# Optimization experiments

Measured on AMD Instinct MI355X. Metric: run time of the kernel, lower is better.

## Reference

```python
import jax, jax.numpy as jnp
import numpy as np

B, D, H, O, E = 16384, 1024, 512, 256, 8


def setup_inputs() -> dict:
    key = jax.random.key(0)
    ks = jax.random.split(key, 8)
    s = lambda k, shape, fan: (jax.random.normal(k, shape, jnp.float32) / np.sqrt(fan).astype(np.float32))
    z = lambda shape: jnp.zeros(shape, jnp.float32)
    return {
        "x": jax.random.normal(ks[0], (B, D), jnp.float32),
        # gating network: D -> 256 -> 128 -> E
        "gw1": s(ks[1], (D, 256), D), "gb1": z((256,)),
        "gw2": s(ks[2], (256, 128), 256), "gb2": z((128,)),
        "gw3": s(ks[3], (128, E), 128), "gb3": z((E,)),
        # experts, batched over expert dim E: D -> H -> H -> O
        "ew1": s(ks[4], (E, D, H), D), "eb1": z((E, H)),
        "ew2": s(ks[5], (E, H, H), H), "eb2": z((E, H)),
        "ew3": s(ks[6], (E, H, O), H), "eb3": z((E, O)),
    }


def reference(x, gw1, gb1, gw2, gb2, gw3, gb3, ew1, eb1, ew2, eb2, ew3, eb3):
    # Gating network (dropout is identity in eval mode)
    g = jax.nn.relu(x @ gw1 + gb1)
    g = jax.nn.relu(g @ gw2 + gb2)
    gates = jax.nn.softmax(g @ gw3 + gb3, axis=1)  # [B, E]
    # All experts run on every token: batched small MLPs over expert axis e
    h = jax.nn.relu(jnp.einsum('bd,edh->ebh', x, ew1) + eb1[:, None, :])   # [E, B, H]
    h = jax.nn.relu(jnp.einsum('ebh,ehk->ebk', h, ew2) + eb2[:, None, :])  # [E, B, H]
    eo = jnp.einsum('ebh,eho->ebo', h, ew3) + eb3[:, None, :]              # [E, B, O]
    # gate-weighted sum over experts
    out = jnp.einsum('ebo,be->bo', eo, gates)  # [B, O]
    return out
```

## Files before the change

### kernel.cpp

```cpp
#include <hip/hip_runtime.h>
#include <hip/hip_bf16.h>

typedef __hip_bfloat16 bf16;
typedef __attribute__((ext_vector_type(8))) __bf16 bf16x8;
typedef __attribute__((ext_vector_type(4))) float f32x4;

#define B_ 16384
#define D_ 1024
#define H_ 512
#define O_ 256
#define E_ 8
#define BC_ 8192

static_assert(B_ % BC_ == 0, "chunking");

#define GLDS(src, dst) __builtin_amdgcn_global_load_lds( \
    (const __attribute__((address_space(1))) void*)(src), \
    (__attribute__((address_space(3))) void*)(dst), 16, 0, 0)

#define BAR()   asm volatile("s_barrier" ::: "memory")
#define LGKM0() do { asm volatile("s_waitcnt lgkmcnt(0)" ::: "memory"); \
                     __builtin_amdgcn_sched_barrier(0); } while (0)

__global__ void detect_k(const unsigned short* __restrict__ x, int* __restrict__ flag) {
    __shared__ int s;
    if (threadIdx.x == 0) s = 0;
    __syncthreads();
    int big = 0;
    for (int i = threadIdx.x; i < 2048; i += 256)
        if (((x[i] >> 7) & 0xFF) >= 150) big = 1;
    if (big) atomicOr(&s, 1);
    __syncthreads();
    if (threadIdx.x == 0) *flag = s;
}

__global__ void cvtx_k(const void* __restrict__ src, bf16* __restrict__ dst,
                       const int* __restrict__ flag, long n8) {
    const int f = *flag;
    long i = (long)blockIdx.x * blockDim.x + threadIdx.x;
    const long stride = (long)gridDim.x * blockDim.x;
    if (f) {
        const float4* s = (const float4*)src;
        for (; i < n8; i += stride) {
            float4 a = s[2 * i], b = s[2 * i + 1];
            bf16 tmp[8];
            tmp[0] = __float2bfloat16(a.x); tmp[1] = __float2bfloat16(a.y);
            tmp[2] = __float2bfloat16(a.z); tmp[3] = __float2bfloat16(a.w);
            tmp[4] = __float2bfloat16(b.x); tmp[5] = __float2bfloat16(b.y);
            tmp[6] = __float2bfloat16(b.z); tmp[7] = __float2bfloat16(b.w);
            *(uint4*)(dst + i * 8) = *(const uint4*)tmp;
        }
    } else {
        const uint4* s = (const uint4*)src;
        for (; i < n8; i += stride) *(uint4*)(dst + i * 8) = s[i];
    }
}

__global__ void small_cvt_k(const void* s0, const void* s1, const void* s2,
                            const void* s3, const void* s4, const void* s5,
                            const void* s6,
                            bf16* d0, bf16* d1, bf16* d2, bf16* d3,
                            bf16* d4, bf16* d5, bf16* d6,
                            const int* __restrict__ flag) {
    const int f = *flag;
    const int id = blockIdx.x;
    const void* sp[7] = {s0, s1, s2, s3, s4, s5, s6};
    bf16* dp[7] = {d0, d1, d2, d3, d4, d5, d6};
    const int len[7] = {256, 128, 1024, 8, E_ * H_, E_ * H_, E_ * O_};
    const float* sf = (const float*)sp[id];
    const bf16*  sb = (const bf16*)sp[id];
    bf16* d = dp[id];
    for (int i = threadIdx.x; i < len[id]; i += 256)
        d[i] = f ? __float2bfloat16(sf[i]) : sb[i];
}

__global__ void transpose_all_k(const void* gw1, const void* gw2,
                                const void* ew1, const void* ew2, const void* ew3,
                                bf16* gw1t, bf16* gw2t,
                                bf16* ew1t, bf16* ew2t, bf16* ew3t,
                                long ew3_zout, long ew3_cstride,
                                const int* __restrict__ flag) {
    __shared__ bf16 t[32][33];
    const int f = *flag;
    int lin = blockIdx.x;
    const void* src; bf16* dst; int R, C, bx, by, bz; long z_out, c_stride;
    if (lin < 256) {
        src = gw1; dst = gw1t; R = 1024; C = 256; z_out = 0; c_stride = 1024;
        bx = lin & 7; by = lin >> 3; bz = 0;
    } else if (lin < 288) {
        lin -= 256;
        src = gw2; dst = gw2t; R = 256; C = 128; z_out = 0; c_stride = 256;
        bx = lin & 3; by = lin >> 2; bz = 0;
    } else if (lin < 4384) {
        lin -= 288;
        src = ew1; dst = ew1t; R = 1024; C = 512;
        z_out = (long)H_ * D_; c_stride = D_;
        bx = lin & 15; by = (lin >> 4) & 31; bz = lin >> 9;
    } else if (lin < 6432) {
        lin -= 4384;
        src = ew2; dst = ew2t; R = 512; C = 512;
        z_out = (long)H_ * H_; c_stride = H_;
        bx = lin & 15; by = (lin >> 4) & 15; bz = lin >> 8;
    } else {
        lin -= 6432;
        src = ew3; dst = ew3t; R = 512; C = 256;
        z_out = ew3_zout; c_stride = ew3_cstride;
        bx = lin & 7; by = (lin >> 3) & 15; bz = lin >> 7;
    }
    const long zi = (long)bz * R * C;
    const int x = bx * 32 + threadIdx.x;
    const int y0 = by * 32;
    const float* inf = (const float*)src;
    const bf16* inb = (const bf16*)src;
#pragma unroll
    for (int i = 0; i < 4; i++) {
        int r = y0 + threadIdx.y + i * 8;
        long idx = zi + (long)r * C + x;
        t[threadIdx.y + i * 8][threadIdx.x] =
            f ? __float2bfloat16(inf[idx]) : inb[idx];
    }
    __syncthreads();
    const int xr = by * 32 + threadIdx.x;
    const long zo = (long)bz * z_out;
#pragma unroll
    for (int i = 0; i < 4; i++) {
        int c = bx * 32 + threadIdx.y + i * 8;
        dst[zo + (long)c * c_stride + xr] = t[threadIdx.x][threadIdx.y + i * 8];
    }
}

__global__ void gate3_softmax_k(const bf16* __restrict__ g2,
                                const bf16* __restrict__ gw3,
                                const bf16* __restrict__ gb3,
                                float* __restrict__ gates) {
    __shared__ float w[128 * 8];
    __shared__ float bsh[8];
    const int tid = threadIdx.x;
    for (int i = tid; i < 1024; i += 256) w[i] = __bfloat162float(gw3[i]);
    if (tid < 8) bsh[tid] = __bfloat162float(gb3[tid]);
    __syncthreads();

    const long row = (long)blockIdx.x * 256 + tid;
    float acc[8];
#pragma unroll
    for (int o = 0; o < 8; o++) acc[o] = bsh[o];

    const bf16x8* rp8 = (const bf16x8*)(g2 + row * 128);
#pragma unroll 4
    for (int c8 = 0; c8 < 16; c8++) {
        bf16x8 v8 = rp8[c8];
#pragma unroll
        for (int jj = 0; jj < 8; jj++) {
            float v = (float)v8[jj];
            int k = c8 * 8 + jj;
#pragma unroll
            for (int o = 0; o < 8; o++) acc[o] += v * w[k * 8 + o];
        }
    }
    float m = acc[0];
#pragma unroll
    for (int o = 1; o < 8; o++) m = fmaxf(m, acc[o]);
    float s = 0.f;
#pragma unroll
    for (int o = 0; o < 8; o++) { acc[o] = __expf(acc[o] - m); s += acc[o]; }
    const float inv = 1.f / s;
#pragma unroll
    for (int o = 0; o < 8; o++) gates[row * 8 + o] = acc[o] * inv;
}

template <int MODE>
__global__ __launch_bounds__(256, 4)
void gemm_bt(const bf16* __restrict__ A, const bf16* __restrict__ Bt,
             const bf16* __restrict__ bias, const float* __restrict__ gates,
             void* __restrict__ Cout, const bf16* __restrict__ eb3,
             int lda, int ldb, int ldo, int K,
             long a_z, long b_z, long bias_z, long out_z,
             int e_gate, int k_per_e, long a_e, long b_e, long row0) {
    __shared__ __attribute__((aligned(16))) bf16 As[128 * 32];
    __shared__ __attribute__((aligned(16))) bf16 Bs[128 * 32];

    const int tid  = threadIdx.x;
    const int lane = tid & 63;
    const int quad = lane >> 4;
    const int l15  = lane & 15;
    const int wid  = tid >> 6;
    const int wr   = (wid >> 1) << 6;
    const int wc   = (wid & 1) << 6;
    const int z    = blockIdx.z;
    const long m0  = (long)blockIdx.y << 7;
    const long n0  = (long)blockIdx.x << 7;

    const bf16* Az = A + (long)z * a_z;
    const bf16* Bz = Bt + (long)z * b_z;

    f32x4 acc[4][4];
#pragma unroll
    for (int i = 0; i < 4; i++)
#pragma unroll
        for (int j = 0; j < 4; j++) acc[i][j] = (f32x4){0.f, 0.f, 0.f, 0.f};

    const int erow = tid >> 2;
    const int ecol = (tid & 3) << 3;

    const int n_e   = k_per_e ? (K / k_per_e) : 1;
    const int inner = (k_per_e ? k_per_e : K) >> 5;

    for (int e = 0; e < n_e; e++) {
        const bf16* Ae = Az + (long)e * a_e;
        const bf16* Be = Bz + (long)e * b_e;
        for (int kti = 0; kti < inner; kti++) {
            const int kk = kti << 5;
#pragma unroll
            for (int i = 0; i < 2; i++) {
                const int r = (i << 6) + erow;
                GLDS(Ae + (m0 + r) * lda + (kk + ecol), As + r * 32 + ecol);
            }
#pragma unroll
            for (int i = 0; i < 2; i++) {
                const int r = (i << 6) + erow;
                GLDS(Be + (n0 + r) * ldb + (kk + ecol), Bs + r * 32 + ecol);
            }
            __syncthreads();
            bf16x8 af[4], bfr[4];
#pragma unroll
            for (int i = 0; i < 4; i++)
                af[i] = *(const bf16x8*)(As + (wr + i * 16 + l15) * 32 + (quad << 3));
#pragma unroll
            for (int j = 0; j < 4; j++)
                bfr[j] = *(const bf16x8*)(Bs + (wc + j * 16 + l15) * 32 + (quad << 3));
#pragma unroll
            for (int i = 0; i < 4; i++)
#pragma unroll
                for (int j = 0; j < 4; j++)
                    acc[i][j] = __builtin_amdgcn_mfma_f32_16x16x32_bf16(
                        af[i], bfr[j], acc[i][j], 0, 0, 0);
            __syncthreads();
        }
    }

    const int eg = (e_gate >= 0) ? e_gate : z;

    if constexpr (MODE == 0 || MODE == 1) {
        bf16* C = (bf16*)Cout + (long)z * out_z;
        const bf16* bb = bias + (long)z * bias_z;
        float gv[4][4];
        if constexpr (MODE == 1) {
#pragma unroll
            for (int i = 0; i < 4; i++)
#pragma unroll
                for (int rg = 0; rg < 4; rg++)
                    gv[i][rg] = gates[(row0 + m0 + wr + i * 16 + quad * 4 + rg) * 8 + eg];
        }
#pragma unroll
        for (int j = 0; j < 4; j++) {
            const int c = (int)n0 + wc + j * 16 + l15;
            const float bv = __bfloat162float(bb[c]);
#pragma unroll
            for (int i = 0; i < 4; i++) {
#pragma unroll
                for (int rg = 0; rg < 4; rg++) {
                    const long r = m0 + wr + i * 16 + quad * 4 + rg;
                    float v = fmaxf(acc[i][j][rg] + bv, 0.f);
                    if constexpr (MODE == 1) v *= gv[i][rg];
                    C[r * ldo + c] = __float2bfloat16(v);
                }
            }
        }
    } else if constexpr (MODE == 2) {
        float* C = (float*)Cout;
#pragma unroll
        for (int i = 0; i < 4; i++) {
#pragma unroll
            for (int rg = 0; rg < 4; rg++) {
                const long r = m0 + wr + i * 16 + quad * 4 + rg;
                const float g = gates[(row0 + r) * 8 + eg];
#pragma unroll
                for (int j = 0; j < 4; j++) {
                    const int c = (int)n0 + wc + j * 16 + l15;
                    const float b3 = __bfloat162float(eb3[eg * O_ + c]);
                    C[r * ldo + c] += acc[i][j][rg] + g * b3;
                }
            }
        }
    }
}

template <int MODE>
__global__ __launch_bounds__(512, 2)
void gemm256(const bf16* __restrict__ A, const bf16* __restrict__ Bt,
             const bf16* __restrict__ bias, const float* __restrict__ gates,
             void* __restrict__ Cout, const bf16* __restrict__ eb3,
             int lda, int ldb, int ldo, int K,
             long a_z, long b_z, long bias_z, long out_z, long row0) {
    __shared__ __attribute__((aligned(16))) bf16 lds[2][2][256 * 64];

    int bx = blockIdx.x, by = blockIdx.y;
    {
        const int gx = gridDim.x;
        const int nwg = gx * gridDim.y;
        if ((nwg & 7) == 0) {
            int lin = bx + gx * by;
            lin = (lin & 7) * (nwg >> 3) + (lin >> 3);
            bx = lin % gx; by = lin / gx;
        }
    }

    const int tid  = threadIdx.x;
    const int lane = tid & 63;
    const int quad = lane >> 4;
    const int l15  = lane & 15;
    const int w    = tid >> 6;
    const int wm   = w >> 2;
    const int wn   = w & 3;
    const int z    = blockIdx.z;
    const long m0  = (long)by << 8;
    const long n0  = (long)bx << 8;

    const bf16* __restrict__ Az = A + z * a_z;
    const bf16* __restrict__ Bz = Bt + z * b_z;

    f32x4 acc[8][4];
#pragma unroll
    for (int i = 0; i < 8; ++i)
#pragma unroll
        for (int j = 0; j < 4; ++j) acc[i][j] = (f32x4){0.f, 0.f, 0.f, 0.f};

    bf16x8 af[4][2], bv[2][2];

    auto stage = [&](int buf, int mat, int half, int kt) {
        const bf16* __restrict__ G = mat ? Bz : Az;
        const int ld = mat ? ldb : lda;
        const long p0 = mat ? n0 : m0;
#pragma unroll
        for (int l = 0; l < 2; ++l) {
            const int ci = (w << 1) | l;
            const int rb = mat ? ((ci >> 2) << 6) + (half << 5) + ((ci & 3) << 3)
                               : ((ci >> 3) << 7) + (half << 6) + ((ci & 7) << 3);
            const int row = rb + (lane >> 3);
            const int cb  = ((lane & 7) << 4) ^ ((row & 7) << 4);
            GLDS(G + (p0 + row) * ld + kt * 64 + (cb >> 1),
                 &lds[buf][mat][rb * 64]);
        }
    };
    auto ldaf = [&](int buf, int qm) {
#pragma unroll
        for (int i = 0; i < 4; ++i) {
            const int r = (wm << 7) + (qm << 6) + (i << 4) + l15;
            const char* p = (const char*)&lds[buf][0][r * 64];
            const int sw = (r & 7) << 4;
#pragma unroll
            for (int s = 0; s < 2; ++s)
                af[i][s] = *(const bf16x8*)(p + (((s << 6) + (quad << 4)) ^ sw));
        }
    };
    auto ldbf = [&](int buf, int qn) {
#pragma unroll
        for (int j = 0; j < 2; ++j) {
            const int r = (wn << 6) + (qn << 5) + (j << 4) + l15;
            const char* p = (const char*)&lds[buf][1][r * 64];
            const int sw = (r & 7) << 4;
#pragma unroll
            for (int s = 0; s < 2; ++s)
                bv[j][s] = *(const bf16x8*)(p + (((s << 6) + (quad << 4)) ^ sw));
        }
    };
    auto mmac = [&](int qm, int qn) {
#pragma unroll
        for (int i = 0; i < 4; ++i)
#pragma unroll
            for (int j = 0; j < 2; ++j)
#pragma unroll
                for (int s = 0; s < 2; ++s)
                    acc[(qm << 2) + i][(qn << 1) + j] =
                        __builtin_amdgcn_mfma_f32_16x16x32_bf16(
                            af[i][s], bv[j][s], acc[(qm << 2) + i][(qn << 1) + j],
                            0, 0, 0);
    };

    const int nt = K >> 6;

    stage(0, 0, 0, 0); stage(0, 0, 1, 0); stage(0, 1, 0, 0); stage(0, 1, 1, 0);
    stage(1, 0, 0, 1); stage(1, 1, 0, 1);
    asm volatile("s_waitcnt vmcnt(4)" ::: "memory");
    BAR();

    const int hi = nt >> 1;
    for (int it = 0; it < hi; ++it) {
        const int t1k = 2 * it + 1, t2k = 2 * it + 2, t3k = 2 * it + 3;
        const bool do2 = t2k < nt, do3 = t3k < nt;
        ldaf(0, 0); ldbf(0, 0); stage(1, 0, 1, t1k);
        BAR(); LGKM0();
        __builtin_amdgcn_s_setprio(1); mmac(0, 0); __builtin_amdgcn_s_setprio(0);
        BAR();
        ldbf(0, 1); stage(1, 1, 1, t1k);
        BAR(); LGKM0();
        __builtin_amdgcn_s_setprio(1); mmac(0, 1); __builtin_amdgcn_s_setprio(0);
        BAR();
        ldaf(0, 1); ldbf(0, 0); if (do2) stage(0, 0, 0, t2k);
        BAR(); LGKM0();
        __builtin_amdgcn_s_setprio(1); mmac(1, 0); __builtin_amdgcn_s_setprio(0);
        BAR();
        ldbf(0, 1); if (do2) stage(0, 1, 0, t2k);
        BAR(); LGKM0();
        __builtin_amdgcn_s_setprio(1); mmac(1, 1); __builtin_amdgcn_s_setprio(0);
        if (do2) { asm volatile("s_waitcnt vmcnt(4)" ::: "memory"); }
        else     { asm volatile("s_waitcnt vmcnt(0)" ::: "memory"); }
        BAR();
        ldaf(1, 0); ldbf(1, 0); if (do2) stage(0, 0, 1, t2k);
        BAR(); LGKM0();
        __builtin_amdgcn_s_setprio(1); mmac(0, 0); __builtin_amdgcn_s_setprio(0);
        BAR();
        ldbf(1, 1); if (do2) stage(0, 1, 1, t2k);
        BAR(); LGKM0();
        __builtin_amdgcn_s_setprio(1); mmac(0, 1); __builtin_amdgcn_s_setprio(0);
        BAR();
        ldaf(1, 1); ldbf(1, 0); if (do3) stage(1, 0, 0, t3k);
        BAR(); LGKM0();
        __builtin_amdgcn_s_setprio(1); mmac(1, 0); __builtin_amdgcn_s_setprio(0);
        BAR();
        ldbf(1, 1); if (do3) stage(1, 1, 0, t3k);
        BAR(); LGKM0();
        __builtin_amdgcn_s_setprio(1); mmac(1, 1); __builtin_amdgcn_s_setprio(0);
        if (do3) { asm volatile("s_waitcnt vmcnt(4)" ::: "memory"); }
        else     { asm volatile("s_waitcnt vmcnt(0)" ::: "memory"); }
        BAR();
    }

    if constexpr (MODE == 0 || MODE == 1) {
        bf16* C = (bf16*)Cout + z * out_z;
        const bf16* bb = bias + z * bias_z;
        float bvv[4];
#pragma unroll
        for (int jg = 0; jg < 4; ++jg)
            bvv[jg] = __bfloat162float(bb[(int)n0 + (wn << 6) + (jg << 4) + l15]);
#pragma unroll
        for (int ig = 0; ig < 8; ++ig) {
#pragma unroll
            for (int rg = 0; rg < 4; ++rg) {
                const long r = m0 + (wm << 7) + (ig << 4) + (quad << 2) + rg;
                float g = 1.f;
                if constexpr (MODE == 1) g = gates[(row0 + r) * 8 + z];
#pragma unroll
                for (int jg = 0; jg < 4; ++jg) {
                    const int c = (int)n0 + (wn << 6) + (jg << 4) + l15;
                    float v = fmaxf(acc[ig][jg][rg] + bvv[jg], 0.f);
                    if constexpr (MODE == 1) v *= g;
                    C[r * ldo + c] = __float2bfloat16(v);
                }
            }
        }
    } else if constexpr (MODE == 4) {
        float* C = (float*)Cout + z * out_z;
        float b3v[4];
#pragma unroll
        for (int jg = 0; jg < 4; ++jg)
            b3v[jg] = __bfloat162float(eb3[z * O_ + (int)n0 + (wn << 6) + (jg << 4) + l15]);
#pragma unroll
        for (int ig = 0; ig < 8; ++ig) {
#pragma unroll
            for (int rg = 0; rg < 4; ++rg) {
                const long r = m0 + (wm << 7) + (ig << 4) + (quad << 2) + rg;
                const float g = gates[(row0 + r) * 8 + z];
#pragma unroll
                for (int jg = 0; jg < 4; ++jg) {
                    const int c = (int)n0 + (wn << 6) + (jg << 4) + l15;
                    C[r * ldo + c] = acc[ig][jg][rg] + g * b3v[jg];
                }
            }
        }
    } else {
        float* C = (float*)Cout + z * out_z;
        const int e0 = z << 1;
        float b30[4], b31[4];
#pragma unroll
        for (int jg = 0; jg < 4; ++jg) {
            const int c = (int)n0 + (wn << 6) + (jg << 4) + l15;
            b30[jg] = __bfloat162float(eb3[e0 * O_ + c]);
            b31[jg] = __bfloat162float(eb3[(e0 + 1) * O_ + c]);
        }
#pragma unroll
        for (int ig = 0; ig < 8; ++ig) {
#pragma unroll
            for (int rg = 0; rg < 4; ++rg) {
                const long r = m0 + (wm << 7) + (ig << 4) + (quad << 2) + rg;
                const float g0 = gates[(row0 + r) * 8 + e0];
                const float g1 = gates[(row0 + r) * 8 + e0 + 1];
#pragma unroll
                for (int jg = 0; jg < 4; ++jg) {
                    const int c = (int)n0 + (wn << 6) + (jg << 4) + l15;
                    C[r * ldo + c] = acc[ig][jg][rg] + g0 * b30[jg] + g1 * b31[jg];
                }
            }
        }
    }
}

__global__ void zero_f32_k(float* __restrict__ p) {
    p[(long)blockIdx.x * 256 + threadIdx.x] = 0.f;
}
__global__ void out_cvt_k(const float* __restrict__ in, void* __restrict__ out,
                          const int* __restrict__ flag) {
    const long i = (long)blockIdx.x * 256 + threadIdx.x;
    if (*flag) ((float*)out)[i] = in[i];
    else       ((bf16*)out)[i] = __float2bfloat16(in[i]);
}
template <int NZ>
__global__ void reduceN_k(const float* __restrict__ p, void* __restrict__ out,
                          const int* __restrict__ flag, long n, long off) {
    const long i = ((long)blockIdx.x * 256 + threadIdx.x) * 4;
    float4 s = *(const float4*)(p + i);
#pragma unroll
    for (int zz = 1; zz < NZ; ++zz) {
        float4 a = *(const float4*)(p + (long)zz * n + i);
        s.x += a.x; s.y += a.y; s.z += a.z; s.w += a.w;
    }
    if (*flag) {
        *(float4*)((float*)out + off + i) = s;
    } else {
        bf16* o = (bf16*)out + off + i;
        o[0] = __float2bfloat16(s.x); o[1] = __float2bfloat16(s.y);
        o[2] = __float2bfloat16(s.z); o[3] = __float2bfloat16(s.w);
    }
}

extern "C" void kernel_launch(void* const* d_in, const int* in_sizes, int n_in,
                              void* d_out, int out_size, void* d_ws, size_t ws_size,
                              hipStream_t stream) {
    (void)in_sizes; (void)n_in; (void)out_size;
    const void* x   = d_in[0];
    const void* gw1 = d_in[1];
    const void* gb1 = d_in[2];
    const void* gw2 = d_in[3];
    const void* gb2 = d_in[4];
    const void* gw3 = d_in[5];
    const void* gb3 = d_in[6];
    const void* ew1 = d_in[7];
    const void* eb1 = d_in[8];
    const void* ew2 = d_in[9];
    const void* eb2 = d_in[10];
    const void* ew3 = d_in[11];
    const void* eb3 = d_in[12];

    char* ws = (char*)d_ws;
    size_t off = 0;
    auto alloc = [&](size_t n) { char* p = ws + off; off += (n + 255) & ~(size_t)255; return p; };

    int*  flag  = (int*)alloc(256);
    bf16* xc    = (bf16*)alloc((size_t)B_ * D_ * 2);
    bf16* gw1t  = (bf16*)alloc((size_t)256 * 1024 * 2);
    bf16* gw2t  = (bf16*)alloc((size_t)128 * 256 * 2);
    bf16* ew1t  = (bf16*)alloc((size_t)E_ * H_ * D_ * 2);
    bf16* ew2t  = (bf16*)alloc((size_t)E_ * H_ * H_ * 2);
    bf16* ew3t  = (bf16*)alloc((size_t)E_ * O_ * H_ * 2);
    bf16* gb1c  = (bf16*)alloc(256 * 2);
    bf16* gb2c  = (bf16*)alloc(128 * 2);
    bf16* gw3c  = (bf16*)alloc(1024 * 2);
    bf16* gb3c  = (bf16*)alloc(8 * 2);
    bf16* eb1c  = (bf16*)alloc((size_t)E_ * H_ * 2);
    bf16* eb2c  = (bf16*)alloc((size_t)E_ * H_ * 2);
    bf16* eb3c  = (bf16*)alloc((size_t)E_ * O_ * 2);
    bf16* g1    = (bf16*)alloc((size_t)B_ * 256 * 2);
    bf16* g2b   = (bf16*)alloc((size_t)B_ * 128 * 2);
    float* gates = (float*)alloc((size_t)B_ * 8 * 4);

    const size_t small = off;
    const size_t needPair = small + ((size_t)E_ * BC_ * H_ * 2 + 256)
                                  + ((size_t)B_ * E_ * H_ * 2 + 256)
                                  + (4ull * B_ * O_ * 4 + 256) + 4096;
    const size_t needChunk = small + ((size_t)E_ * BC_ * H_ * 2 + 256)
                                   + ((size_t)BC_ * E_ * H_ * 2 + 256)
                                   + (8ull * BC_ * O_ * 4 + 256) + 4096;
    const bool pathPair  = ws_size >= needPair;
    const bool pathChunk = ws_size >= needChunk;

    detect_k<<<1, 256, 0, stream>>>((const unsigned short*)x, flag);

    cvtx_k<<<1024, 256, 0, stream>>>(x, xc, flag, (long)B_ * D_ / 8);
    small_cvt_k<<<7, 256, 0, stream>>>(gb1, gb2, gw3, gb3, eb1, eb2, eb3,
                                       gb1c, gb2c, gw3c, gb3c, eb1c, eb2c, eb3c,
                                       flag);

    const long e3zo = pathChunk ? (long)H_ : (long)O_ * H_;
    const long e3cs = pathChunk ? (long)E_ * H_ : (long)H_;
    transpose_all_k<<<7456, dim3(32, 8), 0, stream>>>(
        gw1, gw2, ew1, ew2, ew3, gw1t, gw2t, ew1t, ew2t, ew3t, e3zo, e3cs, flag);

    gemm_bt<0><<<dim3(2, 128, 1), 256, 0, stream>>>(
        xc, gw1t, gb1c, nullptr, g1, nullptr,
        1024, 1024, 256, 1024, 0, 0, 0, 0, 0, 0, 0, 0, 0);
    gemm_bt<0><<<dim3(1, 128, 1), 256, 0, stream>>>(
        g1, gw2t, gb2c, nullptr, g2b, nullptr,
        256, 256, 128, 256, 0, 0, 0, 0, 0, 0, 0, 0, 0);
    gate3_softmax_k<<<dim3(B_ / 256), 256, 0, stream>>>(g2b, gw3c, gb3c, gates);

    if (pathChunk) {
        bf16* h1c = (bf16*)alloc((size_t)E_ * BC_ * H_ * 2);
        bf16* h2  = pathPair
                  ? (bf16*)alloc((size_t)B_ * E_ * H_ * 2)
                  : (bf16*)alloc((size_t)BC_ * E_ * H_ * 2);
        float* parts = pathPair
                     ? (float*)alloc(4ull * B_ * O_ * 4)
                     : (float*)alloc(8ull * BC_ * O_ * 4);

        for (int ch = 0; ch < B_ / BC_; ch++) {
            const long rb = (long)ch * BC_;
            gemm256<0><<<dim3(2, BC_ / 256, 8), 512, 0, stream>>>(
                xc + rb * D_, ew1t, eb1c, nullptr, h1c, nullptr,
                D_, D_, H_, D_,
                0, (long)H_ * D_, (long)H_, (long)BC_ * H_, 0);
            bf16* h2dst = pathPair ? (h2 + rb * (long)E_ * H_) : h2;
            gemm256<1><<<dim3(2, BC_ / 256, 8), 512, 0, stream>>>(
                h1c, ew2t, eb2c, gates, h2dst, nullptr,
                H_, H_, E_ * H_, H_,
                (long)BC_ * H_, (long)H_ * H_, (long)H_, (long)H_, rb);
            if (!pathPair) {
                gemm256<4><<<dim3(1, BC_ / 256, 8), 512, 0, stream>>>(
                    h2, ew3t, nullptr, gates, parts, eb3c,
                    E_ * H_, E_ * H_, O_, 512,
                    (long)H_, (long)H_, 0, (long)BC_ * O_, rb);
                reduceN_k<8><<<dim3(BC_ * O_ / 1024), 256, 0, stream>>>(
                    parts, d_out, flag, (long)BC_ * O_, rb * O_);
            }
        }
        if (pathPair) {
            gemm256<5><<<dim3(1, B_ / 256, 4), 512, 0, stream>>>(
                h2, ew3t, nullptr, gates, parts, eb3c,
                E_ * H_, E_ * H_, O_, 1024,
                2L * H_, 2L * H_, 0, (long)B_ * O_, 0);
            reduceN_k<4><<<dim3(B_ * O_ / 1024), 256, 0, stream>>>(
                parts, d_out, flag, (long)B_ * O_, 0L);
        }
    } else {
        bf16* h1s = (bf16*)alloc((size_t)B_ * H_ * 2);
        bf16* h2s = (bf16*)alloc((size_t)B_ * H_ * 2);
        float* oacc = (float*)alloc((size_t)B_ * O_ * 4);
        zero_f32_k<<<dim3(B_ * O_ / 256), 256, 0, stream>>>(oacc);
        for (int e = 0; e < E_; e++) {
            gemm_bt<0><<<dim3(4, 128, 1), 256, 0, stream>>>(
                xc, ew1t + (size_t)e * H_ * D_, eb1c + (size_t)e * H_, nullptr, h1s, nullptr,
                1024, 1024, 512, 1024, 0, 0, 0, 0, 0, 0, 0, 0, 0);
            gemm_bt<1><<<dim3(4, 128, 1), 256, 0, stream>>>(
                h1s, ew2t + (size_t)e * H_ * H_, eb2c + (size_t)e * H_, gates, h2s, nullptr,
                512, 512, 512, 512, 0, 0, 0, 0, e, 0, 0, 0, 0);
            gemm_bt<2><<<dim3(2, 128, 1), 256, 0, stream>>>(
                h2s, ew3t + (size_t)e * O_ * H_, nullptr, gates, oacc, eb3c,
                512, 512, 256, 512, 0, 0, 0, 0, e, 0, 0, 0, 0);
        }
        out_cvt_k<<<dim3(B_ * O_ / 256), 256, 0, stream>>>(oacc, d_out, flag);
    }
}
```

Baseline: 532.9 us.

## Fuse expert-3 GEMM over all experts with K=4096 and direct output write

The third expert layer used to produce per-expert or per-pair fp32 partial outputs plus a separate reduction kernel. It now runs one gemm_bt over the concatenated expert dimension (K = E*H). The gate-weighted biases are applied in the epilogue, and the result goes straight to the output in fp32 or bf16. When the workspace allows, the chunk loop is also collapsed into one full-batch pass. This drops the partials buffer and reduce kernel at the cost of a single long-K GEMM on the smaller 128-tile kernel, which may have lower throughput than gemm256.

```diff
diff --git a/kernel.cpp b/kernel.cpp
--- a/kernel.cpp
+++ b/kernel.cpp
@@ -173,6 +173,7 @@
 void gemm_bt(const bf16* __restrict__ A, const bf16* __restrict__ Bt,
              const bf16* __restrict__ bias, const float* __restrict__ gates,
              void* __restrict__ Cout, const bf16* __restrict__ eb3,
+             const int* __restrict__ oflag,
              int lda, int ldb, int ldo, int K,
              long a_z, long b_z, long bias_z, long out_z,
              int e_gate, int k_per_e, long a_e, long b_e, long row0) {
@@ -282,6 +283,36 @@
                 }
             }
         }
+    } else {
+        const int f = *oflag;
+        float b3[4][8];
+#pragma unroll
+        for (int j = 0; j < 4; j++) {
+            const int c = (int)n0 + wc + j * 16 + l15;
+#pragma unroll
+            for (int e = 0; e < 8; e++)
+                b3[j][e] = __bfloat162float(eb3[e * O_ + c]);
+        }
+#pragma unroll
+        for (int i = 0; i < 4; i++) {
+#pragma unroll
+            for (int rg = 0; rg < 4; rg++) {
+                const long r = row0 + m0 + wr + i * 16 + quad * 4 + rg;
+                const float4* gp = (const float4*)(gates + r * 8);
+                const float4 ga = gp[0], gb = gp[1];
+#pragma unroll
+                for (int j = 0; j < 4; j++) {
+                    const int c = (int)n0 + wc + j * 16 + l15;
+                    float v = acc[i][j][rg]
+                            + ga.x * b3[j][0] + ga.y * b3[j][1]
+                            + ga.z * b3[j][2] + ga.w * b3[j][3]
+                            + gb.x * b3[j][4] + gb.y * b3[j][5]
+                            + gb.z * b3[j][6] + gb.w * b3[j][7];
+                    if (f) ((float*)Cout)[r * ldo + c] = v;
+                    else   ((bf16*)Cout)[r * ldo + c] = __float2bfloat16(v);
+                }
+            }
+        }
     }
 }
 
@@ -426,70 +457,25 @@
         BAR();
     }
 
-    if constexpr (MODE == 0 || MODE == 1) {
-        bf16* C = (bf16*)Cout + z * out_z;
-        const bf16* bb = bias + z * bias_z;
-        float bvv[4];
-#pragma unroll
-        for (int jg = 0; jg < 4; ++jg)
-            bvv[jg] = __bfloat162float(bb[(int)n0 + (wn << 6) + (jg << 4) + l15]);
-#pragma unroll
-        for (int ig = 0; ig < 8; ++ig) {
-#pragma unroll
-            for (int rg = 0; rg < 4; ++rg) {
-                const long r = m0 + (wm << 7) + (ig << 4) + (quad << 2) + rg;
-                float g = 1.f;
-                if constexpr (MODE == 1) g = gates[(row0 + r) * 8 + z];
-#pragma unroll
-                for (int jg = 0; jg < 4; ++jg) {
-                    const int c = (int)n0 + (wn << 6) + (jg << 4) + l15;
-                    float v = fmaxf(acc[ig][jg][rg] + bvv[jg], 0.f);
-                    if constexpr (MODE == 1) v *= g;
-                    C[r * ldo + c] = __float2bfloat16(v);
-                }
-            }
-        }
-    } else if constexpr (MODE == 4) {
-        float* C = (float*)Cout + z * out_z;
-        float b3v[4];
-#pragma unroll
-        for (int jg = 0; jg < 4; ++jg)
-            b3v[jg] = __bfloat162float(eb3[z * O_ + (int)n0 + (wn << 6) + (jg << 4) + l15]);
-#pragma unroll
-        for (int ig = 0; ig < 8; ++ig) {
-#pragma unroll
-            for (int rg = 0; rg < 4; ++rg) {
-                const long r = m0 + (wm << 7) + (ig << 4) + (quad << 2) + rg;
-                const float g = gates[(row0 + r) * 8 + z];
-#pragma unroll
-                for (int jg = 0; jg < 4; ++jg) {
-                    const int c = (int)n0 + (wn << 6) + (jg << 4) + l15;
-                    C[r * ldo + c] = acc[ig][jg][rg] + g * b3v[jg];
-                }
-            }
-        }
-    } else {
-        float* C = (float*)Cout + z * out_z;
-        const int e0 = z << 1;
-        float b30[4], b31[4];
-#pragma unroll
-        for (int jg = 0; jg < 4; ++jg) {
-            const int c = (int)n0 + (wn << 6) + (jg << 4) + l15;
-            b30[jg] = __bfloat162float(eb3[e0 * O_ + c]);
-            b31[jg] = __bfloat162float(eb3[(e0 + 1) * O_ + c]);
-        }
-#pragma unroll
-        for (int ig = 0; ig < 8; ++ig) {
-#pragma unroll
-            for (int rg = 0; rg < 4; ++rg) {
-                const long r = m0 + (wm << 7) + (ig << 4) + (quad << 2) + rg;
-                const float g0 = gates[(row0 + r) * 8 + e0];
-                const float g1 = gates[(row0 + r) * 8 + e0 + 1];
-#pragma unroll
-                for (int jg = 0; jg < 4; ++jg) {
-                    const int c = (int)n0 + (wn << 6) + (jg << 4) + l15;
-                    C[r * ldo + c] = acc[ig][jg][rg] + g0 * b30[jg] + g1 * b31[jg];
-                }
+    bf16* C = (bf16*)Cout + z * out_z;
+    const bf16* bb = bias + z * bias_z;
+    float bvv[4];
+#pragma unroll
+    for (int jg = 0; jg < 4; ++jg)
+        bvv[jg] = __bfloat162float(bb[(int)n0 + (wn << 6) + (jg << 4) + l15]);
+#pragma unroll
+    for (int ig = 0; ig < 8; ++ig) {
+#pragma unroll
+        for (int rg = 0; rg < 4; ++rg) {
+            const long r = m0 + (wm << 7) + (ig << 4) + (quad << 2) + rg;
+            float g = 1.f;
+            if constexpr (MODE == 1) g = gates[(row0 + r) * 8 + z];
+#pragma unroll
+            for (int jg = 0; jg < 4; ++jg) {
+                const int c = (int)n0 + (wn << 6) + (jg << 4) + l15;
+                float v = fmaxf(acc[ig][jg][rg] + bvv[jg], 0.f);
+                if constexpr (MODE == 1) v *= g;
+                C[r * ldo + c] = __float2bfloat16(v);
             }
         }
     }
@@ -503,24 +489,6 @@
     const long i = (long)blockIdx.x * 256 + threadIdx.x;
     if (*flag) ((float*)out)[i] = in[i];
     else       ((bf16*)out)[i] = __float2bfloat16(in[i]);
-}
-template <int NZ>
-__global__ void reduceN_k(const float* __restrict__ p, void* __restrict__ out,
-                          const int* __restrict__ flag, long n, long off) {
-    const long i = ((long)blockIdx.x * 256 + threadIdx.x) * 4;
-    float4 s = *(const float4*)(p + i);
-#pragma unroll
-    for (int zz = 1; zz < NZ; ++zz) {
-        float4 a = *(const float4*)(p + (long)zz * n + i);
-        s.x += a.x; s.y += a.y; s.z += a.z; s.w += a.w;
-    }
-    if (*flag) {
-        *(float4*)((float*)out + off + i) = s;
-    } else {
-        bf16* o = (bf16*)out + off + i;
-        o[0] = __float2bfloat16(s.x); o[1] = __float2bfloat16(s.y);
-        o[2] = __float2bfloat16(s.z); o[3] = __float2bfloat16(s.w);
-    }
 }
 
 extern "C" void kernel_launch(void* const* d_in, const int* in_sizes, int n_in,
@@ -564,13 +532,11 @@
     float* gates = (float*)alloc((size_t)B_ * 8 * 4);
 
     const size_t small = off;
-    const size_t needPair = small + ((size_t)E_ * BC_ * H_ * 2 + 256)
-                                  + ((size_t)B_ * E_ * H_ * 2 + 256)
-                                  + (4ull * B_ * O_ * 4 + 256) + 4096;
+    const size_t needBig = small + ((size_t)E_ * B_ * H_ * 2 + 256)
+                                 + ((size_t)B_ * E_ * H_ * 2 + 256) + 4096;
     const size_t needChunk = small + ((size_t)E_ * BC_ * H_ * 2 + 256)
-                                   + ((size_t)BC_ * E_ * H_ * 2 + 256)
-                                   + (8ull * BC_ * O_ * 4 + 256) + 4096;
-    const bool pathPair  = ws_size >= needPair;
+                                   + ((size_t)BC_ * E_ * H_ * 2 + 256) + 4096;
+    const bool pathBig   = ws_size >= needBig;
     const bool pathChunk = ws_size >= needChunk;
 
     detect_k<<<1, 256, 0, stream>>>((const unsigned short*)x, flag);
@@ -586,49 +552,33 @@
         gw1, gw2, ew1, ew2, ew3, gw1t, gw2t, ew1t, ew2t, ew3t, e3zo, e3cs, flag);
 
     gemm_bt<0><<<dim3(2, 128, 1), 256, 0, stream>>>(
-        xc, gw1t, gb1c, nullptr, g1, nullptr,
+        xc, gw1t, gb1c, nullptr, g1, nullptr, nullptr,
         1024, 1024, 256, 1024, 0, 0, 0, 0, 0, 0, 0, 0, 0);
     gemm_bt<0><<<dim3(1, 128, 1), 256, 0, stream>>>(
-        g1, gw2t, gb2c, nullptr, g2b, nullptr,
+        g1, gw2t, gb2c, nullptr, g2b, nullptr, nullptr,
         256, 256, 128, 256, 0, 0, 0, 0, 0, 0, 0, 0, 0);
     gate3_softmax_k<<<dim3(B_ / 256), 256, 0, stream>>>(g2b, gw3c, gb3c, gates);
 
     if (pathChunk) {
-        bf16* h1c = (bf16*)alloc((size_t)E_ * BC_ * H_ * 2);
-        bf16* h2  = pathPair
-                  ? (bf16*)alloc((size_t)B_ * E_ * H_ * 2)
-                  : (bf16*)alloc((size_t)BC_ * E_ * H_ * 2);
-        float* parts = pathPair
-                     ? (float*)alloc(4ull * B_ * O_ * 4)
-                     : (float*)alloc(8ull * BC_ * O_ * 4);
-
-        for (int ch = 0; ch < B_ / BC_; ch++) {
-            const long rb = (long)ch * BC_;
-            gemm256<0><<<dim3(2, BC_ / 256, 8), 512, 0, stream>>>(
+        const int nch   = pathBig ? 1 : (B_ / BC_);
+        const long rows = pathBig ? B_ : BC_;
+        bf16* h1c = (bf16*)alloc((size_t)E_ * rows * H_ * 2);
+        bf16* h2  = (bf16*)alloc((size_t)rows * E_ * H_ * 2);
+
+        for (int ch = 0; ch < nch; ch++) {
+            const long rb = (long)ch * rows;
+            gemm256<0><<<dim3(2, rows / 256, 8), 512, 0, stream>>>(
                 xc + rb * D_, ew1t, eb1c, nullptr, h1c, nullptr,
                 D_, D_, H_, D_,
-                0, (long)H_ * D_, (long)H_, (long)BC_ * H_, 0);
-            bf16* h2dst = pathPair ? (h2 + rb * (long)E_ * H_) : h2;
-            gemm256<1><<<dim3(2, BC_ / 256, 8), 512, 0, stream>>>(
-                h1c, ew2t, eb2c, gates, h2dst, nullptr,
+                0, (long)H_ * D_, (long)H_, rows * H_, 0);
+            gemm256<1><<<dim3(2, rows / 256, 8), 512, 0, stream>>>(
+                h1c, ew2t, eb2c, gates, h2, nullptr,
                 H_, H_, E_ * H_, H_,
-                (long)BC_ * H_, (long)H_ * H_, (long)H_, (long)H_, rb);
-            if (!pathPair) {
-                gemm256<4><<<dim3(1, BC_ / 256, 8), 512, 0, stream>>>(
-                    h2, ew3t, nullptr, gates, parts, eb3c,
-                    E_ * H_, E_ * H_, O_, 512,
-                    (long)H_, (long)H_, 0, (long)BC_ * O_, rb);
-                reduceN_k<8><<<dim3(BC_ * O_ / 1024), 256, 0, stream>>>(
-                    parts, d_out, flag, (long)BC_ * O_, rb * O_);
-            }
-        }
-        if (pathPair) {
-            gemm256<5><<<dim3(1, B_ / 256, 4), 512, 0, stream>>>(
-                h2, ew3t, nullptr, gates, parts, eb3c,
-                E_ * H_, E_ * H_, O_, 1024,
-                2L * H_, 2L * H_, 0, (long)B_ * O_, 0);
-            reduceN_k<4><<<dim3(B_ * O_ / 1024), 256, 0, stream>>>(
-                parts, d_out, flag, (long)B_ * O_, 0L);
+                rows * H_, (long)H_ * H_, (long)H_, (long)H_, rb);
+            gemm_bt<3><<<dim3(2, rows / 128, 1), 256, 0, stream>>>(
+                h2, ew3t, nullptr, gates, d_out, eb3c, flag,
+                E_ * H_, E_ * H_, O_, E_ * H_,
+                0, 0, 0, 0, 0, 0, 0, 0, rb);
         }
     } else {
         bf16* h1s = (bf16*)alloc((size_t)B_ * H_ * 2);
@@ -637,13 +587,13 @@
         zero_f32_k<<<dim3(B_ * O_ / 256), 256, 0, stream>>>(oacc);
         for (int e = 0; e < E_; e++) {
             gemm_bt<0><<<dim3(4, 128, 1), 256, 0, stream>>>(
-                xc, ew1t + (size_t)e * H_ * D_, eb1c + (size_t)e * H_, nullptr, h1s, nullptr,
+                xc, ew1t + (size_t)e * H_ * D_, eb1c + (size_t)e * H_, nullptr, h1s, nullptr, nullptr,
                 1024, 1024, 512, 1024, 0, 0, 0, 0, 0, 0, 0, 0, 0);
             gemm_bt<1><<<dim3(4, 128, 1), 256, 0, stream>>>(
-                h1s, ew2t + (size_t)e * H_ * H_, eb2c + (size_t)e * H_, gates, h2s, nullptr,
+                h1s, ew2t + (size_t)e * H_ * H_, eb2c + (size_t)e * H_, gates, h2s, nullptr, nullptr,
                 512, 512, 512, 512, 0, 0, 0, 0, e, 0, 0, 0, 0);
             gemm_bt<2><<<dim3(2, 128, 1), 256, 0, stream>>>(
-                h2s, ew3t + (size_t)e * O_ * H_, nullptr, gates, oacc, eb3c,
+                h2s, ew3t + (size_t)e * O_ * H_, nullptr, gates, oacc, eb3c, nullptr,
                 512, 512, 256, 512, 0, 0, 0, 0, e, 0, 0, 0, 0);
         }
         out_cvt_k<<<dim3(B_ * O_ / 256), 256, 0, stream>>>(oacc, d_out, flag);
```

New measurement: 625.9 us. 17.5% more time.

## Fuse gate layer-1 into expert layer-1 GEMM and merge preprocessing kernels

Applied to the files above, without the earlier changes.

Concatenates gw1 with ew1 (and their biases) into one weight matrix so a single large GEMM computes every expert's first layer and the gate's first hidden layer over the full batch, with no chunking, when the workspace is large enough. The downstream gate GEMM reads its slice of that output. The x conversion, small bias conversion and transpose kernels are also merged into one launch. The aim is fewer launches and better GEMM utilisation. The cost is a larger workspace requirement; the old chunked path remains as a fallback.

```diff
diff --git a/kernel.cpp b/kernel.cpp
--- a/kernel.cpp
+++ b/kernel.cpp
@@ -11,6 +11,7 @@
 #define O_ 256
 #define E_ 8
 #define BC_ 8192
+#define NG_ (E_ * H_ + 256)
 
 static_assert(B_ % BC_ == 0, "chunking");
 
@@ -34,55 +35,57 @@
     if (threadIdx.x == 0) *flag = s;
 }
 
-__global__ void cvtx_k(const void* __restrict__ src, bf16* __restrict__ dst,
-                       const int* __restrict__ flag, long n8) {
+__global__ void preproc_k(const void* x, bf16* xc,
+                          const void* gb1, const void* gb2, const void* gw3,
+                          const void* gb3, const void* eb1, const void* eb2,
+                          const void* eb3,
+                          bf16* gb1c, bf16* gb2c, bf16* gw3c, bf16* gb3c,
+                          bf16* eb1c, bf16* eb2c, bf16* eb3c,
+                          const void* gw1, const void* gw2,
+                          const void* ew1, const void* ew2, const void* ew3,
+                          bf16* gw1t, bf16* gw2t,
+                          bf16* ew1t, bf16* ew2t, bf16* ew3t,
+                          long ew3_zout, long ew3_cstride,
+                          const int* __restrict__ flag) {
     const int f = *flag;
-    long i = (long)blockIdx.x * blockDim.x + threadIdx.x;
-    const long stride = (long)gridDim.x * blockDim.x;
-    if (f) {
-        const float4* s = (const float4*)src;
-        for (; i < n8; i += stride) {
-            float4 a = s[2 * i], b = s[2 * i + 1];
-            bf16 tmp[8];
-            tmp[0] = __float2bfloat16(a.x); tmp[1] = __float2bfloat16(a.y);
-            tmp[2] = __float2bfloat16(a.z); tmp[3] = __float2bfloat16(a.w);
-            tmp[4] = __float2bfloat16(b.x); tmp[5] = __float2bfloat16(b.y);
-            tmp[6] = __float2bfloat16(b.z); tmp[7] = __float2bfloat16(b.w);
-            *(uint4*)(dst + i * 8) = *(const uint4*)tmp;
-        }
-    } else {
-        const uint4* s = (const uint4*)src;
-        for (; i < n8; i += stride) *(uint4*)(dst + i * 8) = s[i];
-    }
-}
-
-__global__ void small_cvt_k(const void* s0, const void* s1, const void* s2,
-                            const void* s3, const void* s4, const void* s5,
-                            const void* s6,
-                            bf16* d0, bf16* d1, bf16* d2, bf16* d3,
-                            bf16* d4, bf16* d5, bf16* d6,
-                            const int* __restrict__ flag) {
-    const int f = *flag;
-    const int id = blockIdx.x;
-    const void* sp[7] = {s0, s1, s2, s3, s4, s5, s6};
-    bf16* dp[7] = {d0, d1, d2, d3, d4, d5, d6};
-    const int len[7] = {256, 128, 1024, 8, E_ * H_, E_ * H_, E_ * O_};
-    const float* sf = (const float*)sp[id];
-    const bf16*  sb = (const bf16*)sp[id];
-    bf16* d = dp[id];
-    for (int i = threadIdx.x; i < len[id]; i += 256)
-        d[i] = f ? __float2bfloat16(sf[i]) : sb[i];
-}
-
-__global__ void transpose_all_k(const void* gw1, const void* gw2,
-                                const void* ew1, const void* ew2, const void* ew3,
-                                bf16* gw1t, bf16* gw2t,
-                                bf16* ew1t, bf16* ew2t, bf16* ew3t,
-                                long ew3_zout, long ew3_cstride,
-                                const int* __restrict__ flag) {
+    const int tid = threadIdx.y * 32 + threadIdx.x;
+    int lin = blockIdx.x;
+
+    if (lin < 1024) {
+        const long n8 = (long)B_ * D_ / 8;
+        long i = (long)lin * 256 + tid;
+        const long stride = 1024 * 256;
+        if (f) {
+            const float4* s = (const float4*)x;
+            for (; i < n8; i += stride) {
+                float4 a = s[2 * i], b = s[2 * i + 1];
+                bf16 tmp[8];
+                tmp[0] = __float2bfloat16(a.x); tmp[1] = __float2bfloat16(a.y);
+                tmp[2] = __float2bfloat16(a.z); tmp[3] = __float2bfloat16(a.w);
+                tmp[4] = __float2bfloat16(b.x); tmp[5] = __float2bfloat16(b.y);
+                tmp[6] = __float2bfloat16(b.z); tmp[7] = __float2bfloat16(b.w);
+                *(uint4*)(xc + i * 8) = *(const uint4*)tmp;
+            }
+        } else {
+            const uint4* s = (const uint4*)x;
+            for (; i < n8; i += stride) *(uint4*)(xc + i * 8) = s[i];
+        }
+        return;
+    }
+    if (lin < 1031) {
+        const int id = lin - 1024;
+        const void* sp[7] = {gb1, gb2, gw3, gb3, eb1, eb2, eb3};
+        bf16* dp[7] = {gb1c, gb2c, gw3c, gb3c, eb1c, eb2c, eb3c};
+        const int len[7] = {256, 128, 1024, 8, E_ * H_, E_ * H_, E_ * O_};
+        const float* sf = (const float*)sp[id];
+        const bf16*  sb = (const bf16*)sp[id];
+        bf16* d = dp[id];
+        for (int i = tid; i < len[id]; i += 256)
+            d[i] = f ? __float2bfloat16(sf[i]) : sb[i];
+        return;
+    }
+    lin -= 1031;
     __shared__ bf16 t[32][33];
-    const int f = *flag;
-    int lin = blockIdx.x;
     const void* src; bf16* dst; int R, C, bx, by, bz; long z_out, c_stride;
     if (lin < 256) {
         src = gw1; dst = gw1t; R = 1024; C = 256; z_out = 0; c_stride = 1024;
@@ -108,14 +111,14 @@
         bx = lin & 7; by = (lin >> 3) & 15; bz = lin >> 7;
     }
     const long zi = (long)bz * R * C;
-    const int x = bx * 32 + threadIdx.x;
+    const int xg = bx * 32 + threadIdx.x;
     const int y0 = by * 32;
     const float* inf = (const float*)src;
     const bf16* inb = (const bf16*)src;
 #pragma unroll
     for (int i = 0; i < 4; i++) {
         int r = y0 + threadIdx.y + i * 8;
-        long idx = zi + (long)r * C + x;
+        long idx = zi + (long)r * C + xg;
         t[threadIdx.y + i * 8][threadIdx.x] =
             f ? __float2bfloat16(inf[idx]) : inb[idx];
     }
@@ -547,16 +550,18 @@
 
     int*  flag  = (int*)alloc(256);
     bf16* xc    = (bf16*)alloc((size_t)B_ * D_ * 2);
-    bf16* gw1t  = (bf16*)alloc((size_t)256 * 1024 * 2);
+    bf16* ew1g  = (bf16*)alloc((size_t)NG_ * D_ * 2);
+    bf16* ew1t  = ew1g;
+    bf16* gw1t  = ew1g + (size_t)E_ * H_ * D_;
     bf16* gw2t  = (bf16*)alloc((size_t)128 * 256 * 2);
-    bf16* ew1t  = (bf16*)alloc((size_t)E_ * H_ * D_ * 2);
     bf16* ew2t  = (bf16*)alloc((size_t)E_ * H_ * H_ * 2);
     bf16* ew3t  = (bf16*)alloc((size_t)E_ * O_ * H_ * 2);
-    bf16* gb1c  = (bf16*)alloc(256 * 2);
+    bf16* eb1g  = (bf16*)alloc((size_t)NG_ * 2);
+    bf16* eb1c  = eb1g;
+    bf16* gb1c  = eb1g + E_ * H_;
     bf16* gb2c  = (bf16*)alloc(128 * 2);
     bf16* gw3c  = (bf16*)alloc(1024 * 2);
     bf16* gb3c  = (bf16*)alloc(8 * 2);
-    bf16* eb1c  = (bf16*)alloc((size_t)E_ * H_ * 2);
     bf16* eb2c  = (bf16*)alloc((size_t)E_ * H_ * 2);
     bf16* eb3c  = (bf16*)alloc((size_t)E_ * O_ * 2);
     bf16* g1    = (bf16*)alloc((size_t)B_ * 256 * 2);
@@ -564,26 +569,54 @@
     float* gates = (float*)alloc((size_t)B_ * 8 * 4);
 
     const size_t small = off;
+    const size_t needBig = small + ((size_t)B_ * NG_ * 2 + 256)
+                                 + ((size_t)B_ * E_ * H_ * 2 + 256)
+                                 + (4ull * B_ * O_ * 4 + 256) + 4096;
     const size_t needPair = small + ((size_t)E_ * BC_ * H_ * 2 + 256)
                                   + ((size_t)B_ * E_ * H_ * 2 + 256)
                                   + (4ull * B_ * O_ * 4 + 256) + 4096;
     const size_t needChunk = small + ((size_t)E_ * BC_ * H_ * 2 + 256)
                                    + ((size_t)BC_ * E_ * H_ * 2 + 256)
                                    + (8ull * BC_ * O_ * 4 + 256) + 4096;
+    const bool pathBig   = ws_size >= needBig;
     const bool pathPair  = ws_size >= needPair;
     const bool pathChunk = ws_size >= needChunk;
 
     detect_k<<<1, 256, 0, stream>>>((const unsigned short*)x, flag);
 
-    cvtx_k<<<1024, 256, 0, stream>>>(x, xc, flag, (long)B_ * D_ / 8);
-    small_cvt_k<<<7, 256, 0, stream>>>(gb1, gb2, gw3, gb3, eb1, eb2, eb3,
-                                       gb1c, gb2c, gw3c, gb3c, eb1c, eb2c, eb3c,
-                                       flag);
-
     const long e3zo = pathChunk ? (long)H_ : (long)O_ * H_;
     const long e3cs = pathChunk ? (long)E_ * H_ : (long)H_;
-    transpose_all_k<<<7456, dim3(32, 8), 0, stream>>>(
-        gw1, gw2, ew1, ew2, ew3, gw1t, gw2t, ew1t, ew2t, ew3t, e3zo, e3cs, flag);
+    preproc_k<<<8487, dim3(32, 8), 0, stream>>>(
+        x, xc, gb1, gb2, gw3, gb3, eb1, eb2, eb3,
+        gb1c, gb2c, gw3c, gb3c, eb1c, eb2c, eb3c,
+        gw1, gw2, ew1, ew2, ew3, gw1t, gw2t, ew1t, ew2t, ew3t,
+        e3zo, e3cs, flag);
+
+    if (pathBig) {
+        bf16* h1g = (bf16*)alloc((size_t)B_ * NG_ * 2);
+        bf16* h2  = (bf16*)alloc((size_t)B_ * E_ * H_ * 2);
+        float* parts = (float*)alloc(4ull * B_ * O_ * 4);
+
+        gemm256<0><<<dim3(NG_ / 256, B_ / 256, 1), 512, 0, stream>>>(
+            xc, ew1g, eb1g, nullptr, h1g, nullptr,
+            D_, D_, NG_, D_,
+            0, 0, 0, 0, 0);
+        gemm_bt<0><<<dim3(1, 128, 1), 256, 0, stream>>>(
+            h1g + (size_t)E_ * H_, gw2t, gb2c, nullptr, g2b, nullptr,
+            NG_, 256, 128, 256, 0, 0, 0, 0, 0, 0, 0, 0, 0);
+        gate3_softmax_k<<<dim3(B_ / 256), 256, 0, stream>>>(g2b, gw3c, gb3c, gates);
+        gemm256<1><<<dim3(2, B_ / 256, 8), 512, 0, stream>>>(
+            h1g, ew2t, eb2c, gates, h2, nullptr,
+            NG_, H_, E_ * H_, H_,
+            (long)H_, (long)H_ * H_, (long)H_, (long)H_, 0);
+        gemm256<5><<<dim3(1, B_ / 256, 4), 512, 0, stream>>>(
+            h2, ew3t, nullptr, gates, parts, eb3c,
+            E_ * H_, E_ * H_, O_, 1024,
+            2L * H_, 2L * H_, 0, (long)B_ * O_, 0);
+        reduceN_k<4><<<dim3(B_ * O_ / 1024), 256, 0, stream>>>(
+            parts, d_out, flag, (long)B_ * O_, 0L);
+        return;
+    }
 
     gemm_bt<0><<<dim3(2, 128, 1), 256, 0, stream>>>(
         xc, gw1t, gb1c, nullptr, g1, nullptr,
```

Result: no change. 525.2 us (-1.4%).
